# Optimization experiments

Hardware: AMD Instinct MI355X
Metric: run time of the kernel (lower is better)

Reference implementation:

```python
import jax, jax.numpy as jnp
import numpy as np

B = 256
N = 256


def setup_inputs() -> dict:
    key = jax.random.key(0)
    ks = jax.random.split(key, 6)
    X = jax.random.normal(ks[0], (B, N), dtype=jnp.float32)
    context = jax.random.normal(ks[1], (B, N), dtype=jnp.float32)
    W = jax.random.normal(ks[2], (N, N), dtype=jnp.float32) * 0.1
    scale = jnp.ones((1,), dtype=jnp.float32)
    A = jax.random.uniform(ks[3], (N, N), dtype=jnp.float32)
    cl_weight = jax.random.normal(ks[4], (N * N, N), dtype=jnp.float32) * 0.02
    cl_bias = jax.random.normal(ks[5], (N * N,), dtype=jnp.float32) * 0.02
    t = 3
    return {"X": X, "context": context, "W": W, "scale": scale, "A": A,
            "cl_weight": cl_weight, "cl_bias": cl_bias, "t": t}


def reference(X, context, W, scale, A, cl_weight, cl_bias, t):
    # context_L path: context-conditioned adjustment of W, shape [B, N, N]
    Bsz, n = X.shape
    adjust = (context @ cl_weight.T + cl_bias).reshape(Bsz, n, n)
    W_new = adjust + W  # broadcast [N,N] over batch
    # diag term: sum over rows i of (W_new @ A)[b, i, k] = einsum bij,jk->bk
    d = jnp.einsum('bij,jk->bk', W_new, A)
    eye = jnp.eye(n, dtype=X.dtype)
    L = d[:, :, None] * eye - W_new          # diag_embed(d) - W_new, [B,N,N]
    new_context = context * (t / (t + 1)) + X / (t + 1)
    L_T = scale * jnp.swapaxes(L, -1, -2)    # [B,N,N]
    update = jnp.einsum('bn,bnm->bm', X, L_T)  # matmul(X[...,None,:], L_T).squeeze()
    return (update, new_context)
```

## Files before the change

kernel.cpp:

```cpp
#include <hip/hip_runtime.h>

#define N 256
#define NN 65536

typedef __attribute__((ext_vector_type(8))) __bf16 bf16x8;
typedef __attribute__((ext_vector_type(4))) __bf16 bf16x4v;
typedef __attribute__((ext_vector_type(4))) float f32x4;

#define F_PART   0u
#define F_SPART  2097152u
#define F_WSC    2621440u
#define F_SFULL  2621696u
#define F_YADJ   2687232u
#define WS_FLOATS 2752768u

static __device__ __forceinline__ f32x4 mfma16(bf16x8 a, bf16x8 b, f32x4 c) {
  return __builtin_amdgcn_mfma_f32_16x16x32_bf16(a, b, c, 0, 0, 0);
}
static __device__ __forceinline__ bf16x4v pack4(float4 v) {
  bf16x4v r;
  r[0] = (__bf16)v.x; r[1] = (__bf16)v.y; r[2] = (__bf16)v.z; r[3] = (__bf16)v.w;
  return r;
}
static __device__ __forceinline__ bf16x8 pack8(float4 a, float4 b) {
  bf16x8 r;
  r[0] = (__bf16)a.x; r[1] = (__bf16)a.y; r[2] = (__bf16)a.z; r[3] = (__bf16)a.w;
  r[4] = (__bf16)b.x; r[5] = (__bf16)b.y; r[6] = (__bf16)b.z; r[7] = (__bf16)b.w;
  return r;
}

typedef __attribute__((address_space(1))) const unsigned int ga_u32;
typedef __attribute__((address_space(3))) unsigned int ls_u32;
static __device__ __forceinline__ void gload16(const void* g, void* l) {
  __builtin_amdgcn_global_load_lds((ga_u32*)g, (ls_u32*)l, 16, 0, 0);
}

#define BARV(NV)                                                          \
  asm volatile("s_waitcnt vmcnt(" #NV ") lgkmcnt(0)" ::: "memory");       \
  __builtin_amdgcn_s_barrier();                                           \
  __builtin_amdgcn_sched_barrier(0);
#define BARL()                                                            \
  asm volatile("s_waitcnt lgkmcnt(0)" ::: "memory");                      \
  __builtin_amdgcn_s_barrier();                                           \
  __builtin_amdgcn_sched_barrier(0);

__global__ void __launch_bounds__(512) kbig(
    const float* __restrict__ X, const float* __restrict__ ctx,
    const float* __restrict__ W, const float* __restrict__ clb,
    const float* __restrict__ clw, float* __restrict__ ws)
{
  extern __shared__ char smem[];
  float* xl   = (float*)(smem + 131072);
  float* sred = (float*)(smem + 139264);
  float* red  = (float*)(smem + 131072);
  const int t = threadIdx.x;
  const int mt = blockIdx.x >> 5, s = blockIdx.x & 31;
  const int n0 = s * 8, m0g = mt * 32;

  const int lane = t & 63, w = t >> 6;
  const int wb = w * 32, l15 = lane & 15, lhi = lane >> 4;
  const int sw2 = (l15 & 7) << 4;

  bf16x8 af[2][8];
#pragma unroll
  for (int i = 0; i < 2; ++i)
#pragma unroll
    for (int c = 0; c < 8; ++c) {
      const float4* p =
          (const float4*)(ctx + (wb + i * 16 + l15) * N + c * 32 + lhi * 8);
      af[i][c] = pack8(p[0], p[1]);
    }
  if (t < 256) {
    const float4* xp = (const float4*)(X + t * N + n0);
    const float4 x0 = xp[0], x1 = xp[1];
    xl[0 * 256 + t] = x0.x; xl[1 * 256 + t] = x0.y;
    xl[2 * 256 + t] = x0.z; xl[3 * 256 + t] = x0.w;
    xl[4 * 256 + t] = x1.x; xl[5 * 256 + t] = x1.y;
    xl[6 * 256 + t] = x1.z; xl[7 * 256 + t] = x1.w;
  }
  __builtin_amdgcn_sched_barrier(0);

#define ISSUE_T(TT, BUFI)                                                   \
  {                                                                         \
    _Pragma("unroll")                                                       \
    for (int i = 0; i < 4; ++i) {                                           \
      const int rowl = w * 4 + i;                                           \
      const size_t grow = (size_t)((m0g + rowl) * 256 + n0 + (TT));         \
      gload16((const char*)clw + grow * 1024 +                              \
                  (size_t)((lane * 16) ^ ((rowl & 7) << 4)),                \
              smem + (BUFI) * 32768 + rowl * 1024);                         \
    }                                                                       \
  }

  const f32x4 zero = {0.f, 0.f, 0.f, 0.f};
  f32x4 acc[2][2];
  acc[0][0] = zero; acc[0][1] = zero; acc[1][0] = zero; acc[1][1] = zero;

#define COMP(NNV)                                                           \
  {                                                                         \
    const char* buf = smem + ((NNV) & 3) * 32768;                           \
    f32x4 h[2][2];                                                          \
    h[0][0] = zero; h[0][1] = zero; h[1][0] = zero; h[1][1] = zero;         \
    _Pragma("unroll")                                                       \
    for (int c = 0; c < 8; ++c) {                                           \
      const int colb = c * 128 + lhi * 32;                                  \
      const float4 p00 = *(const float4*)(buf + l15 * 1024 + (colb ^ sw2)); \
      const float4 p01 =                                                    \
          *(const float4*)(buf + l15 * 1024 + ((colb + 16) ^ sw2));         \
      const float4 p10 =                                                    \
          *(const float4*)(buf + (16 + l15) * 1024 + (colb ^ sw2));         \
      const float4 p11 =                                                    \
          *(const float4*)(buf + (16 + l15) * 1024 + ((colb + 16) ^ sw2));  \
      const bf16x8 b0 = pack8(p00, p01);                                    \
      const bf16x8 b1 = pack8(p10, p11);                                    \
      h[0][0] = mfma16(af[0][c], b0, h[0][0]);                              \
      h[0][1] = mfma16(af[0][c], b1, h[0][1]);                              \
      h[1][0] = mfma16(af[1][c], b0, h[1][0]);                              \
      h[1][1] = mfma16(af[1][c], b1, h[1][1]);                              \
    }                                                                       \
    _Pragma("unroll")                                                       \
    for (int fb = 0; fb < 2; ++fb) {                                        \
      _Pragma("unroll")                                                     \
      for (int r = 0; r < 4; ++r) {                                         \
        const int brow = wb + fb * 16 + lhi * 4 + r;                        \
        const float xv = xl[(NNV) * 256 + brow];                            \
        acc[fb][0][r] += xv * h[fb][0][r];                                  \
        acc[fb][1][r] += xv * h[fb][1][r];                                  \
        float v = h[fb][0][r] + h[fb][1][r];                                \
        v += __shfl_xor(v, 1); v += __shfl_xor(v, 2);                       \
        v += __shfl_xor(v, 4); v += __shfl_xor(v, 8);                       \
        if (l15 == 0) sred[(NNV) * 256 + brow] = v;                         \
      }                                                                     \
    }                                                                       \
  }

  ISSUE_T(0, 0) ISSUE_T(1, 1) ISSUE_T(2, 2) ISSUE_T(3, 3)
  BARV(12)
  COMP(0) BARL() ISSUE_T(4, 0)
  BARV(12)
  COMP(1) BARL() ISSUE_T(5, 1)
  BARV(12)
  COMP(2) BARL() ISSUE_T(6, 2)
  BARV(12)
  COMP(3) BARL() ISSUE_T(7, 3)
  BARV(12)
  COMP(4) BARL()
  BARV(8)
  COMP(5) BARL()
  BARV(4)
  COMP(6) BARL()
  BARV(0)
  COMP(7)
#undef ISSUE_T
#undef COMP

  const int base = blockIdx.x * 8192;
#pragma unroll
  for (int fb = 0; fb < 2; ++fb)
#pragma unroll
    for (int fm = 0; fm < 2; ++fm)
#pragma unroll
      for (int r = 0; r < 4; ++r)
        ws[F_PART + base + (wb + fb * 16 + lhi * 4 + r) * 32 + fm * 16 + l15] =
            acc[fb][fm][r];

  {
    const int b = wb + (lane >> 1);
    const int nh = (lane & 1) * 4;
    float4 v;
    v.x = sred[(nh + 0) * 256 + b];
    v.y = sred[(nh + 1) * 256 + b];
    v.z = sred[(nh + 2) * 256 + b];
    v.w = sred[(nh + 3) * 256 + b];
    *(float4*)(ws + F_SPART + mt * NN + b * N + n0 + nh) = v;
  }

  if (mt == 0) {
    __syncthreads();
    if (t < 256) {
      const float4* wp = (const float4*)(W + t * N + s * 8);
      const float4* cp = (const float4*)(clb + t * N + s * 8);
      const float4 a0 = wp[0], a1 = wp[1], b0 = cp[0], b1 = cp[1];
      red[0 * 256 + t] = a0.x + b0.x; red[1 * 256 + t] = a0.y + b0.y;
      red[2 * 256 + t] = a0.z + b0.z; red[3 * 256 + t] = a0.w + b0.w;
      red[4 * 256 + t] = a1.x + b1.x; red[5 * 256 + t] = a1.y + b1.y;
      red[6 * 256 + t] = a1.z + b1.z; red[7 * 256 + t] = a1.w + b1.w;
    }
    __syncthreads();
    if (t < 64) {
      const int jj = t >> 3, seg = t & 7;
      float v = 0.f;
#pragma unroll
      for (int i = 0; i < 32; ++i) v += red[jj * 256 + seg * 32 + i];
      v += __shfl_xor(v, 1);
      v += __shfl_xor(v, 2);
      v += __shfl_xor(v, 4);
      if (seg == 0) ws[F_WSC + s * 8 + jj] = v;
    }
  }
}

__global__ void __launch_bounds__(256) kred(float* __restrict__ ws)
{
  const int o = blockIdx.x * 256 + threadIdx.x;
  const int b = o >> 8, col = o & 255;
  const int mt = col >> 5, ml = col & 31;
  float y = 0.f;
#pragma unroll
  for (int si = 0; si < 32; ++si)
    y += ws[F_PART + ((mt * 32 + si) * 256 + b) * 32 + ml];
  ws[F_YADJ + o] = y;
  float sv = ws[F_WSC + col];
#pragma unroll
  for (int q = 0; q < 8; ++q)
    sv += ws[F_SPART + q * NN + o];
  ws[F_SFULL + o] = sv;
}

__global__ void __launch_bounds__(256) kfin(
    const float* __restrict__ X, const float* __restrict__ ctx,
    const float* __restrict__ W, const float* __restrict__ clb,
    const float* __restrict__ A, const float* __restrict__ scale,
    const int* __restrict__ tptr, float* __restrict__ out,
    float* __restrict__ ws)
{
  extern __shared__ char smem[];
  const int t = threadIdx.x, blk = blockIdx.x;
  const int b0 = (blk >> 3) * 32, k0 = (blk & 7) * 32;
  {
    const int row = t >> 3, q = t & 7;
    const int sw = (row & 7) << 4;
    const float4* sp = (const float4*)(ws + F_SFULL + (b0 + row) * N);
    const float4* xp = (const float4*)(X + (b0 + row) * N);
    const float4* wp = (const float4*)(W + (k0 + row) * N);
    const float4* cp = (const float4*)(clb + (k0 + row) * N);
#pragma unroll
    for (int i = 0; i < 8; ++i) {
      const int f4 = q * 8 + i;
      const int off = row * 512 + ((f4 * 8) ^ sw);
      *(bf16x4v*)(smem + off) = pack4(sp[f4]);
      *(bf16x4v*)(smem + 16384 + off) = pack4(xp[f4]);
      const float4 wv = wp[f4], cv = cp[f4];
      float4 s2;
      s2.x = wv.x + cv.x; s2.y = wv.y + cv.y;
      s2.z = wv.z + cv.z; s2.w = wv.w + cv.w;
      *(bf16x4v*)(smem + 49152 + off) = pack4(s2);
    }
    const float4* ap = (const float4*)(A + t * N + k0);
    char* at = smem + 32768;
#pragma unroll
    for (int i = 0; i < 8; ++i) {
      const float4 v = ap[i];
      const int kk = i * 4;
      *(__bf16*)(at + (kk + 0) * 512 + ((t * 2) ^ (((kk + 0) & 7) << 4))) = (__bf16)v.x;
      *(__bf16*)(at + (kk + 1) * 512 + ((t * 2) ^ (((kk + 1) & 7) << 4))) = (__bf16)v.y;
      *(__bf16*)(at + (kk + 2) * 512 + ((t * 2) ^ (((kk + 2) & 7) << 4))) = (__bf16)v.z;
      *(__bf16*)(at + (kk + 3) * 512 + ((t * 2) ^ (((kk + 3) & 7) << 4))) = (__bf16)v.w;
    }
  }
  __syncthreads();
  const int lane = t & 63, w = t >> 6;
  const int l15 = lane & 15, lhi = lane >> 4;
  const int wqb = (w >> 1) * 16, wqk = (w & 1) * 16;
  const int swz = (l15 & 7) << 4;
  f32x4 accd = {0.f, 0.f, 0.f, 0.f}, accw = {0.f, 0.f, 0.f, 0.f};
#pragma unroll
  for (int c = 0; c < 8; ++c) {
    const int kb = c * 64 + lhi * 16;
    bf16x8 as  = *(const bf16x8*)(smem + (wqb + l15) * 512 + (kb ^ swz));
    bf16x8 aat = *(const bf16x8*)(smem + 32768 + (wqk + l15) * 512 + (kb ^ swz));
    bf16x8 ax  = *(const bf16x8*)(smem + 16384 + (wqb + l15) * 512 + (kb ^ swz));
    bf16x8 awc = *(const bf16x8*)(smem + 49152 + (wqk + l15) * 512 + (kb ^ swz));
    accd = mfma16(as, aat, accd);
    accw = mfma16(ax, awc, accw);
  }
  const float sc = scale[0];
  const float tf = (float)(*tptr);
  const float c1 = tf / (tf + 1.f), c2 = 1.f / (tf + 1.f);
#pragma unroll
  for (int r = 0; r < 4; ++r) {
    const int b = b0 + wqb + lhi * 4 + r, k = k0 + wqk + l15;
    const int idx = b * N + k;
    const float xv = X[idx];
    out[idx] = sc * (xv * accd[r] - accw[r] - ws[F_YADJ + idx]);
    out[NN + idx] = ctx[idx] * c1 + xv * c2;
  }
}

extern "C" void kernel_launch(void* const* d_in, const int* in_sizes, int n_in,
                              void* d_out, int out_size, void* d_ws, size_t ws_size,
                              hipStream_t stream)
{
  (void)in_sizes; (void)n_in; (void)out_size;
  const float* X     = (const float*)d_in[0];
  const float* ctx   = (const float*)d_in[1];
  const float* W     = (const float*)d_in[2];
  const float* scale = (const float*)d_in[3];
  const float* A     = (const float*)d_in[4];
  const float* clw   = (const float*)d_in[5];
  const float* clb   = (const float*)d_in[6];
  const int*   tptr  = (const int*)d_in[7];
  float* out = (float*)d_out;
  float* ws  = (float*)d_ws;

  if (ws_size < (size_t)WS_FLOATS * sizeof(float)) return;

  (void)hipFuncSetAttribute((const void*)kbig,
                            hipFuncAttributeMaxDynamicSharedMemorySize, 147456);
  (void)hipFuncSetAttribute((const void*)kfin,
                            hipFuncAttributeMaxDynamicSharedMemorySize, 65536);

  kbig<<<256, 512, 147456, stream>>>(X, ctx, W, clb, clw, ws);
  kred<<<256, 256, 0, stream>>>(ws);
  kfin<<<64, 256, 65536, stream>>>(X, ctx, W, clb, A, scale, tptr, out, ws);
}
```

Measured before the change: 60.97 us.

## Split big kernel over batch halves with double-buffered LDS for two blocks per CU

The main kernel now launches 512 blocks of 256 threads, each handling half the batch (128 rows), instead of 256 blocks of 512 threads. The clw tile ring drops from four LDS buffers to two, so LDS use halves and two blocks can share a CU, and the reduction kernel indexing changes to match the new partial layout. The aim is to fill more CUs and overlap blocks. The cost is that each clw tile is now loaded twice (once per batch half), doubling weight traffic, and the prefetch depth is shallower.

```diff
diff --git a/kernel.cpp b/kernel.cpp
--- a/kernel.cpp
+++ b/kernel.cpp
@@ -44,21 +44,24 @@
   __builtin_amdgcn_s_barrier();                                           \
   __builtin_amdgcn_sched_barrier(0);
 
-__global__ void __launch_bounds__(512) kbig(
+__global__ void __launch_bounds__(256, 2) kbig(
     const float* __restrict__ X, const float* __restrict__ ctx,
     const float* __restrict__ W, const float* __restrict__ clb,
     const float* __restrict__ clw, float* __restrict__ ws)
 {
   extern __shared__ char smem[];
-  float* xl   = (float*)(smem + 131072);
-  float* sred = (float*)(smem + 139264);
-  float* red  = (float*)(smem + 131072);
+  float* xl   = (float*)(smem + 65536);
+  float* sred = (float*)(smem + 69632);
+  float* red  = (float*)smem;
   const int t = threadIdx.x;
-  const int mt = blockIdx.x >> 5, s = blockIdx.x & 31;
-  const int n0 = s * 8, m0g = mt * 32;
+  const int bh = blockIdx.x >> 8;
+  const int rem = blockIdx.x & 255;
+  const int mt = rem >> 5, s = rem & 31;
+  const int n0 = s * 8, m0g = mt * 32, b0g = bh * 128;
 
   const int lane = t & 63, w = t >> 6;
-  const int wb = w * 32, l15 = lane & 15, lhi = lane >> 4;
+  const int wb = w * 32;
+  const int l15 = lane & 15, lhi = lane >> 4;
   const int sw2 = (l15 & 7) << 4;
 
   bf16x8 af[2][8];
@@ -66,25 +69,25 @@
   for (int i = 0; i < 2; ++i)
 #pragma unroll
     for (int c = 0; c < 8; ++c) {
-      const float4* p =
-          (const float4*)(ctx + (wb + i * 16 + l15) * N + c * 32 + lhi * 8);
+      const float4* p = (const float4*)(ctx + (b0g + wb + i * 16 + l15) * N +
+                                        c * 32 + lhi * 8);
       af[i][c] = pack8(p[0], p[1]);
     }
-  if (t < 256) {
-    const float4* xp = (const float4*)(X + t * N + n0);
+  if (t < 128) {
+    const float4* xp = (const float4*)(X + (b0g + t) * N + n0);
     const float4 x0 = xp[0], x1 = xp[1];
-    xl[0 * 256 + t] = x0.x; xl[1 * 256 + t] = x0.y;
-    xl[2 * 256 + t] = x0.z; xl[3 * 256 + t] = x0.w;
-    xl[4 * 256 + t] = x1.x; xl[5 * 256 + t] = x1.y;
-    xl[6 * 256 + t] = x1.z; xl[7 * 256 + t] = x1.w;
+    xl[0 * 128 + t] = x0.x; xl[1 * 128 + t] = x0.y;
+    xl[2 * 128 + t] = x0.z; xl[3 * 128 + t] = x0.w;
+    xl[4 * 128 + t] = x1.x; xl[5 * 128 + t] = x1.y;
+    xl[6 * 128 + t] = x1.z; xl[7 * 128 + t] = x1.w;
   }
   __builtin_amdgcn_sched_barrier(0);
 
 #define ISSUE_T(TT, BUFI)                                                   \
   {                                                                         \
     _Pragma("unroll")                                                       \
-    for (int i = 0; i < 4; ++i) {                                           \
-      const int rowl = w * 4 + i;                                           \
+    for (int i = 0; i < 8; ++i) {                                           \
+      const int rowl = w * 8 + i;                                           \
       const size_t grow = (size_t)((m0g + rowl) * 256 + n0 + (TT));         \
       gload16((const char*)clw + grow * 1024 +                              \
                   (size_t)((lane * 16) ^ ((rowl & 7) << 4)),                \
@@ -98,7 +101,7 @@
 
 #define COMP(NNV)                                                           \
   {                                                                         \
-    const char* buf = smem + ((NNV) & 3) * 32768;                           \
+    const char* buf = smem + ((NNV) & 1) * 32768;                           \
     f32x4 h[2][2];                                                          \
     h[0][0] = zero; h[0][1] = zero; h[1][0] = zero; h[1][1] = zero;         \
     _Pragma("unroll")                                                       \
@@ -123,38 +126,38 @@
       _Pragma("unroll")                                                     \
       for (int r = 0; r < 4; ++r) {                                         \
         const int brow = wb + fb * 16 + lhi * 4 + r;                        \
-        const float xv = xl[(NNV) * 256 + brow];                            \
+        const float xv = xl[(NNV) * 128 + brow];                            \
         acc[fb][0][r] += xv * h[fb][0][r];                                  \
         acc[fb][1][r] += xv * h[fb][1][r];                                  \
         float v = h[fb][0][r] + h[fb][1][r];                                \
         v += __shfl_xor(v, 1); v += __shfl_xor(v, 2);                       \
         v += __shfl_xor(v, 4); v += __shfl_xor(v, 8);                       \
-        if (l15 == 0) sred[(NNV) * 256 + brow] = v;                         \
+        if (l15 == 0) sred[(NNV) * 128 + brow] = v;                         \
       }                                                                     \
     }                                                                       \
   }
 
-  ISSUE_T(0, 0) ISSUE_T(1, 1) ISSUE_T(2, 2) ISSUE_T(3, 3)
-  BARV(12)
-  COMP(0) BARL() ISSUE_T(4, 0)
-  BARV(12)
-  COMP(1) BARL() ISSUE_T(5, 1)
-  BARV(12)
-  COMP(2) BARL() ISSUE_T(6, 2)
-  BARV(12)
-  COMP(3) BARL() ISSUE_T(7, 3)
-  BARV(12)
-  COMP(4) BARL()
-  BARV(8)
-  COMP(5) BARL()
-  BARV(4)
+  ISSUE_T(0, 0) ISSUE_T(1, 1)
+  BARV(8)
+  COMP(0) BARL() ISSUE_T(2, 0)
+  BARV(8)
+  COMP(1) BARL() ISSUE_T(3, 1)
+  BARV(8)
+  COMP(2) BARL() ISSUE_T(4, 0)
+  BARV(8)
+  COMP(3) BARL() ISSUE_T(5, 1)
+  BARV(8)
+  COMP(4) BARL() ISSUE_T(6, 0)
+  BARV(8)
+  COMP(5) BARL() ISSUE_T(7, 1)
+  BARV(8)
   COMP(6) BARL()
   BARV(0)
   COMP(7)
 #undef ISSUE_T
 #undef COMP
 
-  const int base = blockIdx.x * 8192;
+  const int base = blockIdx.x * 4096;
 #pragma unroll
   for (int fb = 0; fb < 2; ++fb)
 #pragma unroll
@@ -165,27 +168,25 @@
             acc[fb][fm][r];
 
   {
-    const int b = wb + (lane >> 1);
+    const int bl = wb + (lane >> 1);
     const int nh = (lane & 1) * 4;
     float4 v;
-    v.x = sred[(nh + 0) * 256 + b];
-    v.y = sred[(nh + 1) * 256 + b];
-    v.z = sred[(nh + 2) * 256 + b];
-    v.w = sred[(nh + 3) * 256 + b];
-    *(float4*)(ws + F_SPART + mt * NN + b * N + n0 + nh) = v;
-  }
-
-  if (mt == 0) {
+    v.x = sred[(nh + 0) * 128 + bl];
+    v.y = sred[(nh + 1) * 128 + bl];
+    v.z = sred[(nh + 2) * 128 + bl];
+    v.w = sred[(nh + 3) * 128 + bl];
+    *(float4*)(ws + F_SPART + mt * NN + (b0g + bl) * N + n0 + nh) = v;
+  }
+
+  if (mt == 0 && bh == 0) {
     __syncthreads();
-    if (t < 256) {
-      const float4* wp = (const float4*)(W + t * N + s * 8);
-      const float4* cp = (const float4*)(clb + t * N + s * 8);
-      const float4 a0 = wp[0], a1 = wp[1], b0 = cp[0], b1 = cp[1];
-      red[0 * 256 + t] = a0.x + b0.x; red[1 * 256 + t] = a0.y + b0.y;
-      red[2 * 256 + t] = a0.z + b0.z; red[3 * 256 + t] = a0.w + b0.w;
-      red[4 * 256 + t] = a1.x + b1.x; red[5 * 256 + t] = a1.y + b1.y;
-      red[6 * 256 + t] = a1.z + b1.z; red[7 * 256 + t] = a1.w + b1.w;
-    }
+    const float4* wp = (const float4*)(W + t * N + s * 8);
+    const float4* cp = (const float4*)(clb + t * N + s * 8);
+    const float4 a0 = wp[0], a1 = wp[1], c0 = cp[0], c1 = cp[1];
+    red[0 * 256 + t] = a0.x + c0.x; red[1 * 256 + t] = a0.y + c0.y;
+    red[2 * 256 + t] = a0.z + c0.z; red[3 * 256 + t] = a0.w + c0.w;
+    red[4 * 256 + t] = a1.x + c1.x; red[5 * 256 + t] = a1.y + c1.y;
+    red[6 * 256 + t] = a1.z + c1.z; red[7 * 256 + t] = a1.w + c1.w;
     __syncthreads();
     if (t < 64) {
       const int jj = t >> 3, seg = t & 7;
@@ -205,10 +206,11 @@
   const int o = blockIdx.x * 256 + threadIdx.x;
   const int b = o >> 8, col = o & 255;
   const int mt = col >> 5, ml = col & 31;
+  const int bhh = b >> 7, bl = b & 127;
   float y = 0.f;
 #pragma unroll
   for (int si = 0; si < 32; ++si)
-    y += ws[F_PART + ((mt * 32 + si) * 256 + b) * 32 + ml];
+    y += ws[F_PART + (bhh * 256 + mt * 32 + si) * 4096 + bl * 32 + ml];
   ws[F_YADJ + o] = y;
   float sv = ws[F_WSC + col];
 #pragma unroll
@@ -306,11 +308,11 @@
   if (ws_size < (size_t)WS_FLOATS * sizeof(float)) return;
 
   (void)hipFuncSetAttribute((const void*)kbig,
-                            hipFuncAttributeMaxDynamicSharedMemorySize, 147456);
+                            hipFuncAttributeMaxDynamicSharedMemorySize, 73728);
   (void)hipFuncSetAttribute((const void*)kfin,
                             hipFuncAttributeMaxDynamicSharedMemorySize, 65536);
 
-  kbig<<<256, 512, 147456, stream>>>(X, ctx, W, clb, clw, ws);
+  kbig<<<512, 256, 73728, stream>>>(X, ctx, W, clb, clw, ws);
   kred<<<256, 256, 0, stream>>>(ws);
   kfin<<<64, 256, 65536, stream>>>(X, ctx, W, clb, A, scale, tptr, out, ws);
 }
```

After: 58.94 us. 1.03x faster.
